# Optimization experiments

Measured on AMD Instinct MI355X. Metric: run time of the kernel, lower is better.

Reference implementation:

```python
import jax, jax.numpy as jnp
import numpy as np

TOP_K = 16
NUM_HEADS = 1
EPS = 1e-8  # torch F.cosine_similarity eps


def setup_inputs() -> dict:
    key = jax.random.key(0)
    ks = jax.random.split(key, 8)
    B, N, Dk, Dv = 64, 8192, 256, 256
    return {
        "query": jax.random.normal(ks[0], (B, Dk), jnp.float32),
        "key_memory": jax.random.normal(ks[1], (B, N, Dk), jnp.float32),
        "value_memory": jax.random.normal(ks[2], (B, N, Dv), jnp.float32),
        "iteration": jax.random.randint(ks[3], (B, 1), 0, N),
        "in_proj_w": jax.random.normal(ks[4], (3 * Dv, Dv), jnp.float32) * 0.06,
        "in_proj_b": jnp.zeros((3 * Dv,), jnp.float32),
        "out_proj_w": jax.random.normal(ks[5], (Dv, Dv), jnp.float32) * 0.06,
        "out_proj_b": jnp.zeros((Dv,), jnp.float32),
    }


def _mha(x, in_w, in_b, out_w, out_b):
    # torch nn.MultiheadAttention (batch_first, qkv same embed dim) self-attention
    B, T, E = x.shape
    H = NUM_HEADS
    hd = E // H
    qkv = x @ in_w.T + in_b                      # [B,T,3E]
    q, k, v = jnp.split(qkv, 3, axis=-1)

    def heads(t):
        return t.reshape(B, T, H, hd).transpose(0, 2, 1, 3)  # [B,H,T,hd]

    q, k, v = heads(q), heads(k), heads(v)
    scale = jnp.asarray(1.0 / np.sqrt(hd), x.dtype)
    attn = jax.nn.softmax(jnp.einsum('bhqd,bhkd->bhqk', q, k) * scale, axis=-1)
    o = jnp.einsum('bhqk,bhkd->bhqd', attn, v).transpose(0, 2, 1, 3).reshape(B, T, E)
    return o @ out_w.T + out_b


def reference(query, key_memory, value_memory, iteration,
              in_proj_w, in_proj_b, out_proj_w, out_proj_b):
    B, N, Dv = value_memory.shape
    # memory validity mask: item n is valid iff n <= iteration[b]
    mem_idx = jnp.arange(N)[None, :]                                   # [1,N]
    mask = (mem_idx <= iteration).astype(key_memory.dtype)[..., None]  # [B,N,1]
    km = key_memory * mask
    vm = value_memory * mask

    # masked cosine similarity between each memory key and the query
    num = jnp.einsum('bnd,bd->bn', km, query)                          # [B,N]
    denom = jnp.maximum(
        jnp.linalg.norm(km, axis=-1) * jnp.linalg.norm(query, axis=-1, keepdims=True),
        EPS)
    sim = num / denom                                                  # [B,N]

    topk_sim, topk_idx = jax.lax.top_k(sim, TOP_K)                     # [B,K]
    topk_vm = jnp.take_along_axis(vm, topk_idx[:, :, None], axis=1)    # [B,K,Dv]

    wv = jax.nn.softmax(topk_sim, axis=-1)[..., None]                  # [B,K,1]
    nrv = wv * topk_vm                                                 # [B,K,Dv]

    nrv = _mha(nrv, in_proj_w, in_proj_b, out_proj_w, out_proj_b)      # [B,K,Dv]

    # rows with iteration == 0 are left as zeros (scatter of computed rows)
    not_first = (iteration.reshape(-1) > 0).astype(nrv.dtype)[:, None, None]
    nrv = nrv * not_first
    return nrv.sum(axis=1)                                             # [B,Dv]
```

## Files before the change

### kernel.cpp

```cpp
#include <hip/hip_runtime.h>
#include <hip/hip_bf16.h>
#include <math.h>

#define B_   64
#define N_   8192
#define D_   256
#define K_   16
#define EPS_ 1e-8f
#define NEG_ -3.4e38f

static const size_t SIM_OFF   = 0;
static const size_t CANDV_OFF = 524288;
static const size_t CANDI_OFF = 655360;
static const size_t QKV_OFF   = 786432;

__global__ void __launch_bounds__(256)
sim_kernel(const float* __restrict__ q, const float* __restrict__ km,
           const int* __restrict__ iter, float* __restrict__ sim) {
    int tid = threadIdx.x;
    int w = tid >> 6, lane = tid & 63;
    int g = lane >> 4, p = lane & 15;
    int seg = (blockIdx.x << 2) + w;
    int b   = seg >> 7;
    int n0  = (seg & 127) << 6;
    int it  = iter[b];
    float* simb = sim + (size_t)b * N_;

    if (n0 > it) { simb[n0 + lane] = 0.f; return; }

    float4 q4[4];
    #pragma unroll
    for (int kk = 0; kk < 4; kk++)
        q4[kk] = *(const float4*)(q + (size_t)b * D_ + kk * 64 + p * 4);
    float qq = q4[0].x*q4[0].x + q4[0].y*q4[0].y + q4[0].z*q4[0].z + q4[0].w*q4[0].w
             + q4[1].x*q4[1].x + q4[1].y*q4[1].y + q4[1].z*q4[1].z + q4[1].w*q4[1].w
             + q4[2].x*q4[2].x + q4[2].y*q4[2].y + q4[2].z*q4[2].z + q4[2].w*q4[2].w
             + q4[3].x*q4[3].x + q4[3].y*q4[3].y + q4[3].z*q4[3].z + q4[3].w*q4[3].w;
    #pragma unroll
    for (int off = 8; off; off >>= 1) qq += __shfl_xor(qq, off);
    float qn = sqrtf(qq);

    const float* kmb = km + (size_t)b * N_ * D_;

    const float* rp0 = kmb + (size_t)min(n0 + g, it) * D_;
    float4 c0 = *(const float4*)(rp0 +   0 + p * 4);
    float4 c1 = *(const float4*)(rp0 +  64 + p * 4);
    float4 c2 = *(const float4*)(rp0 + 128 + p * 4);
    float4 c3 = *(const float4*)(rp0 + 192 + p * 4);

    for (int t = 0; t < 16; t++) {
        int r  = n0 + (t << 2) + g;
        int rn = (t < 15) ? (r + 4) : it;
        const float* rp = kmb + (size_t)min(rn, it) * D_;
        float4 x0 = *(const float4*)(rp +   0 + p * 4);
        float4 x1 = *(const float4*)(rp +  64 + p * 4);
        float4 x2 = *(const float4*)(rp + 128 + p * 4);
        float4 x3 = *(const float4*)(rp + 192 + p * 4);

        float dot = c0.x*q4[0].x + c0.y*q4[0].y + c0.z*q4[0].z + c0.w*q4[0].w
                  + c1.x*q4[1].x + c1.y*q4[1].y + c1.z*q4[1].z + c1.w*q4[1].w
                  + c2.x*q4[2].x + c2.y*q4[2].y + c2.z*q4[2].z + c2.w*q4[2].w
                  + c3.x*q4[3].x + c3.y*q4[3].y + c3.z*q4[3].z + c3.w*q4[3].w;
        float sq  = c0.x*c0.x + c0.y*c0.y + c0.z*c0.z + c0.w*c0.w
                  + c1.x*c1.x + c1.y*c1.y + c1.z*c1.z + c1.w*c1.w
                  + c2.x*c2.x + c2.y*c2.y + c2.z*c2.z + c2.w*c2.w
                  + c3.x*c3.x + c3.y*c3.y + c3.z*c3.z + c3.w*c3.w;
        #pragma unroll
        for (int off = 8; off; off >>= 1) {
            dot += __shfl_xor(dot, off);
            sq  += __shfl_xor(sq,  off);
        }
        float s = (r <= it) ? dot / fmaxf(sqrtf(sq) * qn, EPS_) : 0.f;
        if (p == 0) simb[r] = s;
        c0 = x0; c1 = x1; c2 = x2; c3 = x3;
    }
}

__global__ void __launch_bounds__(256)
cand_kernel(const float* __restrict__ sim,
            float* __restrict__ cand_v, int* __restrict__ cand_i) {
    int tid = threadIdx.x;
    int w = tid >> 6, lane = tid & 63;
    int seg = (blockIdx.x << 2) + w;
    int b   = seg >> 7;
    int n0  = (seg & 127) << 6;
    float v  = sim[(size_t)b * N_ + n0 + lane];
    int  idx = n0 + lane;
    #pragma unroll
    for (int k = 2; k <= 64; k <<= 1) {
        #pragma unroll
        for (int j = k >> 1; j > 0; j >>= 1) {
            float pv = __shfl_xor(v, j);
            int   pi = __shfl_xor(idx, j);
            bool up         = ((lane & k) == 0);
            bool is_lower   = ((lane & j) == 0);
            bool mine_first = (v > pv) || (v == pv && idx < pi);
            bool take_mine  = ((is_lower == up) == mine_first);
            if (!take_mine) { v = pv; idx = pi; }
        }
    }
    if (lane < K_) {
        cand_v[(size_t)seg * K_ + lane] = v;
        cand_i[(size_t)seg * K_ + lane] = idx;
    }
}

__global__ void __launch_bounds__(256)
merge_qkv_kernel(const float* __restrict__ cand_v, const int* __restrict__ cand_i,
                 const float* __restrict__ vm, const int* __restrict__ iter,
                 const float* __restrict__ inw, const float* __restrict__ inb,
                 float* __restrict__ qkv) {
    int bwh = blockIdx.x;
    int b = bwh / 3, which = bwh - b * 3;
    int tid = threadIdx.x, lane = tid & 63;
    int it = iter[b];
    if (it == 0) return;

    __shared__ int   seli[K_];
    __shared__ float scl[K_];
    __shared__ float xs[D_][K_];

    if (tid < 64) {
        float cv[32]; int ci[32];
        #pragma unroll
        for (int j = 0; j < 32; j++) {
            cv[j] = cand_v[(size_t)b * 2048 + (j << 6) + lane];
            ci[j] = cand_i[(size_t)b * 2048 + (j << 6) + lane];
        }
        float selv[K_]; int selidx[K_];
        for (int sel = 0; sel < K_; sel++) {
            float bv = cv[0]; int bi = ci[0];
            #pragma unroll
            for (int j = 1; j < 32; j++)
                if (cv[j] > bv || (cv[j] == bv && ci[j] < bi)) { bv = cv[j]; bi = ci[j]; }
            #pragma unroll
            for (int off = 32; off; off >>= 1) {
                float ov = __shfl_xor(bv, off);
                int   oi = __shfl_xor(bi, off);
                if (ov > bv || (ov == bv && oi < bi)) { bv = ov; bi = oi; }
            }
            #pragma unroll
            for (int j = 0; j < 32; j++)
                if (ci[j] == bi) cv[j] = NEG_;
            selv[sel] = bv; selidx[sel] = bi;
            if (lane == 0) seli[sel] = bi;
        }
        float m = NEG_;
        #pragma unroll
        for (int jj = 0; jj < K_; jj++) m = fmaxf(m, selv[jj]);
        float ssum = 0.f;
        #pragma unroll
        for (int jj = 0; jj < K_; jj++) ssum += expf(selv[jj] - m);
        if (lane < K_) {
            float wgt = expf(selv[lane] - m) / ssum;
            scl[lane] = (selidx[lane] <= it) ? wgt : 0.f;
        }
    }
    __syncthreads();

    #pragma unroll
    for (int kk = 0; kk < K_; kk += 4) {
        float4 px;
        px.x = scl[kk+0] * vm[((size_t)b * N_ + seli[kk+0]) * D_ + tid];
        px.y = scl[kk+1] * vm[((size_t)b * N_ + seli[kk+1]) * D_ + tid];
        px.z = scl[kk+2] * vm[((size_t)b * N_ + seli[kk+2]) * D_ + tid];
        px.w = scl[kk+3] * vm[((size_t)b * N_ + seli[kk+3]) * D_ + tid];
        *(float4*)(&xs[tid][kk]) = px;
    }
    __syncthreads();

    float acc[K_];
    #pragma unroll
    for (int k = 0; k < K_; k++) acc[k] = 0.f;
    const float* wrow = inw + (size_t)(which * D_ + tid) * D_;
    for (int d = 0; d < D_; d += 4) {
        float4 wv4 = *(const float4*)(wrow + d);
        float wk[4] = {wv4.x, wv4.y, wv4.z, wv4.w};
        #pragma unroll
        for (int dd = 0; dd < 4; dd++) {
            float wgt = wk[dd];
            float4 x0 = *(const float4*)(&xs[d + dd][0]);
            float4 x1 = *(const float4*)(&xs[d + dd][4]);
            float4 x2 = *(const float4*)(&xs[d + dd][8]);
            float4 x3 = *(const float4*)(&xs[d + dd][12]);
            acc[0]  += x0.x * wgt; acc[1]  += x0.y * wgt; acc[2]  += x0.z * wgt; acc[3]  += x0.w * wgt;
            acc[4]  += x1.x * wgt; acc[5]  += x1.y * wgt; acc[6]  += x1.z * wgt; acc[7]  += x1.w * wgt;
            acc[8]  += x2.x * wgt; acc[9]  += x2.y * wgt; acc[10] += x2.z * wgt; acc[11] += x2.w * wgt;
            acc[12] += x3.x * wgt; acc[13] += x3.y * wgt; acc[14] += x3.z * wgt; acc[15] += x3.w * wgt;
        }
    }
    float bias = inb[which * D_ + tid];
    #pragma unroll
    for (int k = 0; k < K_; k++)
        qkv[(((size_t)b * 3 + which) * K_ + k) * D_ + tid] = acc[k] + bias;
}

__global__ void __launch_bounds__(256)
attn_out_kernel(const float* __restrict__ qkv, const int* __restrict__ iter,
                const float* __restrict__ ow, const float* __restrict__ ob,
                float* __restrict__ out) {
    int b = blockIdx.x, tid = threadIdx.x;
    int it = iter[b];
    if (it == 0) { out[(size_t)b * D_ + tid] = 0.f; return; }
    __shared__ float qs[K_][260];
    __shared__ float ks[K_][260];
    __shared__ float vs[K_][260];
    __shared__ float attn[K_][K_];
    __shared__ float colsum[K_];
    __shared__ float so[D_];
    const float* base = qkv + (size_t)b * 3 * K_ * D_;
    #pragma unroll
    for (int k = 0; k < K_; k++) {
        qs[k][tid] = base[(0 * K_ + k) * D_ + tid];
        ks[k][tid] = base[(1 * K_ + k) * D_ + tid];
        vs[k][tid] = base[(2 * K_ + k) * D_ + tid];
    }
    __syncthreads();
    int i = tid >> 4, j = tid & 15;
    float s = 0.f;
    for (int d4 = 0; d4 < 64; d4++) {
        float4 qv = *(const float4*)(&qs[i][d4 * 4]);
        float4 kv = *(const float4*)(&ks[j][d4 * 4]);
        s += qv.x*kv.x + qv.y*kv.y + qv.z*kv.z + qv.w*kv.w;
    }
    attn[i][j] = s * 0.0625f;
    __syncthreads();
    if (tid < K_) {
        float m = NEG_;
        for (int jj = 0; jj < K_; jj++) m = fmaxf(m, attn[tid][jj]);
        float ssum = 0.f;
        for (int jj = 0; jj < K_; jj++) ssum += expf(attn[tid][jj] - m);
        float inv = 1.f / ssum;
        for (int jj = 0; jj < K_; jj++) attn[tid][jj] = expf(attn[tid][jj] - m) * inv;
    }
    __syncthreads();
    if (tid < K_) {
        float c = 0.f;
        for (int ii = 0; ii < K_; ii++) c += attn[ii][tid];
        colsum[tid] = c;
    }
    __syncthreads();
    float acc = 0.f;
    #pragma unroll
    for (int jj = 0; jj < K_; jj++) acc += colsum[jj] * vs[jj][tid];
    so[tid] = acc;
    __syncthreads();
    float o = 0.f;
    const float* orow = ow + (size_t)tid * D_;
    for (int e = 0; e < D_; e += 4) {
        float4 wv = *(const float4*)(orow + e);
        float4 sv = *(const float4*)(&so[e]);
        o += sv.x*wv.x + sv.y*wv.y + sv.z*wv.z + sv.w*wv.w;
    }
    out[(size_t)b * D_ + tid] = o + 16.f * ob[tid];
}

extern "C" void kernel_launch(void* const* d_in, const int* in_sizes, int n_in,
                              void* d_out, int out_size, void* d_ws, size_t ws_size,
                              hipStream_t stream) {
    const float* q   = (const float*)d_in[0];
    const float* km  = (const float*)d_in[1];
    const float* vm  = (const float*)d_in[2];
    const int*   it  = (const int*)  d_in[3];
    const float* inw = (const float*)d_in[4];
    const float* inb = (const float*)d_in[5];
    const float* ow  = (const float*)d_in[6];
    const float* ob  = (const float*)d_in[7];
    float* out = (float*)d_out;

    float* ws     = (float*)d_ws;
    float* sim    = ws + SIM_OFF;
    float* cand_v = ws + CANDV_OFF;
    int*   cand_i = (int*)(ws + CANDI_OFF);
    float* qkv    = ws + QKV_OFF;

    sim_kernel<<<dim3(2048), dim3(256), 0, stream>>>(q, km, it, sim);
    cand_kernel<<<dim3(2048), dim3(256), 0, stream>>>(sim, cand_v, cand_i);
    merge_qkv_kernel<<<dim3(B_ * 3), dim3(256), 0, stream>>>(cand_v, cand_i, vm, it, inw, inb, qkv);
    attn_out_kernel<<<dim3(B_), dim3(256), 0, stream>>>(qkv, it, ow, ob, out);
}
```

Measured before the change: 132.8 us.

## Process two key rows per group in sim kernel and split merge from QKV projection

The similarity kernel now handles two memory rows per 16-lane group in each iteration, with more loads in flight, and sets a minimum-occupancy launch bound. The top-k merge and value gather, which the old code ran redundantly in each of the three Q/K/V blocks, now run once per batch row in their own kernel that writes the scaled values to a workspace buffer. A separate QKV projection kernel then reads that buffer from global memory instead of shared memory. This removes the triplicated merge work and adds more memory-level parallelism, at the cost of an extra launch and a global round trip for the gathered values.

Measured after the change: 152.1 us. 14.6% more time.

```diff
diff --git a/kernel.cpp b/kernel.cpp
--- a/kernel.cpp
+++ b/kernel.cpp
@@ -12,9 +12,10 @@
 static const size_t SIM_OFF   = 0;
 static const size_t CANDV_OFF = 524288;
 static const size_t CANDI_OFF = 655360;
-static const size_t QKV_OFF   = 786432;
-
-__global__ void __launch_bounds__(256)
+static const size_t XBUF_OFF  = 786432;
+static const size_t QKV_OFF   = 1048576;
+
+__global__ void __launch_bounds__(256, 4)
 sim_kernel(const float* __restrict__ q, const float* __restrict__ km,
            const int* __restrict__ iter, float* __restrict__ sim) {
     int tid = threadIdx.x;
@@ -41,38 +42,57 @@
     float qn = sqrtf(qq);
 
     const float* kmb = km + (size_t)b * N_ * D_;
-
-    const float* rp0 = kmb + (size_t)min(n0 + g, it) * D_;
-    float4 c0 = *(const float4*)(rp0 +   0 + p * 4);
-    float4 c1 = *(const float4*)(rp0 +  64 + p * 4);
-    float4 c2 = *(const float4*)(rp0 + 128 + p * 4);
-    float4 c3 = *(const float4*)(rp0 + 192 + p * 4);
-
-    for (int t = 0; t < 16; t++) {
-        int r  = n0 + (t << 2) + g;
-        int rn = (t < 15) ? (r + 4) : it;
-        const float* rp = kmb + (size_t)min(rn, it) * D_;
-        float4 x0 = *(const float4*)(rp +   0 + p * 4);
-        float4 x1 = *(const float4*)(rp +  64 + p * 4);
-        float4 x2 = *(const float4*)(rp + 128 + p * 4);
-        float4 x3 = *(const float4*)(rp + 192 + p * 4);
-
-        float dot = c0.x*q4[0].x + c0.y*q4[0].y + c0.z*q4[0].z + c0.w*q4[0].w
-                  + c1.x*q4[1].x + c1.y*q4[1].y + c1.z*q4[1].z + c1.w*q4[1].w
-                  + c2.x*q4[2].x + c2.y*q4[2].y + c2.z*q4[2].z + c2.w*q4[2].w
-                  + c3.x*q4[3].x + c3.y*q4[3].y + c3.z*q4[3].z + c3.w*q4[3].w;
-        float sq  = c0.x*c0.x + c0.y*c0.y + c0.z*c0.z + c0.w*c0.w
-                  + c1.x*c1.x + c1.y*c1.y + c1.z*c1.z + c1.w*c1.w
-                  + c2.x*c2.x + c2.y*c2.y + c2.z*c2.z + c2.w*c2.w
-                  + c3.x*c3.x + c3.y*c3.y + c3.z*c3.z + c3.w*c3.w;
+    int p4 = p * 4;
+
+    float4 a0, a1, a2, a3, b0, b1, b2, b3;
+    {
+        int ra = n0 + (g << 1);
+        const float* pa = kmb + (size_t)min(ra,     it) * D_ + p4;
+        const float* pb = kmb + (size_t)min(ra + 1, it) * D_ + p4;
+        a0 = *(const float4*)(pa);       a1 = *(const float4*)(pa +  64);
+        a2 = *(const float4*)(pa + 128); a3 = *(const float4*)(pa + 192);
+        b0 = *(const float4*)(pb);       b1 = *(const float4*)(pb +  64);
+        b2 = *(const float4*)(pb + 128); b3 = *(const float4*)(pb + 192);
+    }
+
+    for (int t = 0; t < 8; t++) {
+        int ra = n0 + (t << 3) + (g << 1);
+        int nx = (t < 7) ? (ra + 8) : it;
+        const float* pa = kmb + (size_t)min(nx,     it) * D_ + p4;
+        const float* pb = kmb + (size_t)min(nx + 1, it) * D_ + p4;
+        float4 xa0 = *(const float4*)(pa);       float4 xa1 = *(const float4*)(pa +  64);
+        float4 xa2 = *(const float4*)(pa + 128); float4 xa3 = *(const float4*)(pa + 192);
+        float4 xb0 = *(const float4*)(pb);       float4 xb1 = *(const float4*)(pb +  64);
+        float4 xb2 = *(const float4*)(pb + 128); float4 xb3 = *(const float4*)(pb + 192);
+
+        float dota = a0.x*q4[0].x + a0.y*q4[0].y + a0.z*q4[0].z + a0.w*q4[0].w
+                   + a1.x*q4[1].x + a1.y*q4[1].y + a1.z*q4[1].z + a1.w*q4[1].w
+                   + a2.x*q4[2].x + a2.y*q4[2].y + a2.z*q4[2].z + a2.w*q4[2].w
+                   + a3.x*q4[3].x + a3.y*q4[3].y + a3.z*q4[3].z + a3.w*q4[3].w;
+        float sqa  = a0.x*a0.x + a0.y*a0.y + a0.z*a0.z + a0.w*a0.w
+                   + a1.x*a1.x + a1.y*a1.y + a1.z*a1.z + a1.w*a1.w
+                   + a2.x*a2.x + a2.y*a2.y + a2.z*a2.z + a2.w*a2.w
+                   + a3.x*a3.x + a3.y*a3.y + a3.z*a3.z + a3.w*a3.w;
+        float dotb = b0.x*q4[0].x + b0.y*q4[0].y + b0.z*q4[0].z + b0.w*q4[0].w
+                   + b1.x*q4[1].x + b1.y*q4[1].y + b1.z*q4[1].z + b1.w*q4[1].w
+                   + b2.x*q4[2].x + b2.y*q4[2].y + b2.z*q4[2].z + b2.w*q4[2].w
+                   + b3.x*q4[3].x + b3.y*q4[3].y + b3.z*q4[3].z + b3.w*q4[3].w;
+        float sqb  = b0.x*b0.x + b0.y*b0.y + b0.z*b0.z + b0.w*b0.w
+                   + b1.x*b1.x + b1.y*b1.y + b1.z*b1.z + b1.w*b1.w
+                   + b2.x*b2.x + b2.y*b2.y + b2.z*b2.z + b2.w*b2.w
+                   + b3.x*b3.x + b3.y*b3.y + b3.z*b3.z + b3.w*b3.w;
         #pragma unroll
         for (int off = 8; off; off >>= 1) {
-            dot += __shfl_xor(dot, off);
-            sq  += __shfl_xor(sq,  off);
-        }
-        float s = (r <= it) ? dot / fmaxf(sqrtf(sq) * qn, EPS_) : 0.f;
-        if (p == 0) simb[r] = s;
-        c0 = x0; c1 = x1; c2 = x2; c3 = x3;
+            dota += __shfl_xor(dota, off);
+            sqa  += __shfl_xor(sqa,  off);
+            dotb += __shfl_xor(dotb, off);
+            sqb  += __shfl_xor(sqb,  off);
+        }
+        float sa = (ra     <= it) ? dota / fmaxf(sqrtf(sqa) * qn, EPS_) : 0.f;
+        float sb = (ra + 1 <= it) ? dotb / fmaxf(sqrtf(sqb) * qn, EPS_) : 0.f;
+        if (p == 0) { simb[ra] = sa; simb[ra + 1] = sb; }
+        a0 = xa0; a1 = xa1; a2 = xa2; a3 = xa3;
+        b0 = xb0; b1 = xb1; b2 = xb2; b3 = xb3;
     }
 }
 
@@ -106,19 +126,16 @@
 }
 
 __global__ void __launch_bounds__(256)
-merge_qkv_kernel(const float* __restrict__ cand_v, const int* __restrict__ cand_i,
-                 const float* __restrict__ vm, const int* __restrict__ iter,
-                 const float* __restrict__ inw, const float* __restrict__ inb,
-                 float* __restrict__ qkv) {
-    int bwh = blockIdx.x;
-    int b = bwh / 3, which = bwh - b * 3;
+merge_gather_kernel(const float* __restrict__ cand_v, const int* __restrict__ cand_i,
+                    const float* __restrict__ vm, const int* __restrict__ iter,
+                    float* __restrict__ xbuf) {
+    int b = blockIdx.x;
     int tid = threadIdx.x, lane = tid & 63;
     int it = iter[b];
     if (it == 0) return;
 
     __shared__ int   seli[K_];
     __shared__ float scl[K_];
-    __shared__ float xs[D_][K_];
 
     if (tid < 64) {
         float cv[32]; int ci[32];
@@ -158,6 +175,7 @@
     }
     __syncthreads();
 
+    float* xb = xbuf + (size_t)b * (D_ * K_);
     #pragma unroll
     for (int kk = 0; kk < K_; kk += 4) {
         float4 px;
@@ -165,24 +183,35 @@
         px.y = scl[kk+1] * vm[((size_t)b * N_ + seli[kk+1]) * D_ + tid];
         px.z = scl[kk+2] * vm[((size_t)b * N_ + seli[kk+2]) * D_ + tid];
         px.w = scl[kk+3] * vm[((size_t)b * N_ + seli[kk+3]) * D_ + tid];
-        *(float4*)(&xs[tid][kk]) = px;
-    }
-    __syncthreads();
+        *(float4*)(xb + tid * K_ + kk) = px;
+    }
+}
+
+__global__ void __launch_bounds__(256)
+qkv_kernel(const float* __restrict__ xbuf, const int* __restrict__ iter,
+           const float* __restrict__ inw, const float* __restrict__ inb,
+           float* __restrict__ qkv) {
+    int bwh = blockIdx.x;
+    int b = bwh / 3, which = bwh - b * 3;
+    if (iter[b] == 0) return;
+    int tid = threadIdx.x;
 
     float acc[K_];
     #pragma unroll
     for (int k = 0; k < K_; k++) acc[k] = 0.f;
     const float* wrow = inw + (size_t)(which * D_ + tid) * D_;
+    const float* xb   = xbuf + (size_t)b * (D_ * K_);
     for (int d = 0; d < D_; d += 4) {
         float4 wv4 = *(const float4*)(wrow + d);
         float wk[4] = {wv4.x, wv4.y, wv4.z, wv4.w};
         #pragma unroll
         for (int dd = 0; dd < 4; dd++) {
             float wgt = wk[dd];
-            float4 x0 = *(const float4*)(&xs[d + dd][0]);
-            float4 x1 = *(const float4*)(&xs[d + dd][4]);
-            float4 x2 = *(const float4*)(&xs[d + dd][8]);
-            float4 x3 = *(const float4*)(&xs[d + dd][12]);
+            const float* xr = xb + (d + dd) * K_;
+            float4 x0 = *(const float4*)(xr);
+            float4 x1 = *(const float4*)(xr + 4);
+            float4 x2 = *(const float4*)(xr + 8);
+            float4 x3 = *(const float4*)(xr + 12);
             acc[0]  += x0.x * wgt; acc[1]  += x0.y * wgt; acc[2]  += x0.z * wgt; acc[3]  += x0.w * wgt;
             acc[4]  += x1.x * wgt; acc[5]  += x1.y * wgt; acc[6]  += x1.z * wgt; acc[7]  += x1.w * wgt;
             acc[8]  += x2.x * wgt; acc[9]  += x2.y * wgt; acc[10] += x2.z * wgt; acc[11] += x2.w * wgt;
@@ -272,10 +301,12 @@
     float* sim    = ws + SIM_OFF;
     float* cand_v = ws + CANDV_OFF;
     int*   cand_i = (int*)(ws + CANDI_OFF);
+    float* xbuf   = ws + XBUF_OFF;
     float* qkv    = ws + QKV_OFF;
 
     sim_kernel<<<dim3(2048), dim3(256), 0, stream>>>(q, km, it, sim);
     cand_kernel<<<dim3(2048), dim3(256), 0, stream>>>(sim, cand_v, cand_i);
-    merge_qkv_kernel<<<dim3(B_ * 3), dim3(256), 0, stream>>>(cand_v, cand_i, vm, it, inw, inb, qkv);
+    merge_gather_kernel<<<dim3(B_), dim3(256), 0, stream>>>(cand_v, cand_i, vm, it, xbuf);
+    qkv_kernel<<<dim3(B_ * 3), dim3(256), 0, stream>>>(xbuf, it, inw, inb, qkv);
     attn_out_kernel<<<dim3(B_), dim3(256), 0, stream>>>(qkv, it, ow, ob, out);
 }
```

## Use atomic work-stealing persistent waves for similarity computation

Applied to the files above, without the earlier changes.

Replaces the static one-wave-per-segment mapping in the similarity kernel with a persistent grid where each wave grabs segments from a global atomic counter. Segments are interleaved across batches so that the uneven, iteration-dependent work (segments beyond the valid range exit early) is spread evenly across waves. This adds an init kernel launch, atomic traffic, and a per-segment reload of the query vector.

Result: slower. 238.6 us (+79.7%).

```diff
diff --git a/kernel.cpp b/kernel.cpp
--- a/kernel.cpp
+++ b/kernel.cpp
@@ -6,6 +6,7 @@
 #define N_   8192
 #define D_   256
 #define K_   16
+#define NSEG_ 8192
 #define EPS_ 1e-8f
 #define NEG_ -3.4e38f
 
@@ -13,66 +14,80 @@
 static const size_t CANDV_OFF = 524288;
 static const size_t CANDI_OFF = 655360;
 static const size_t QKV_OFF   = 786432;
+static const size_t CTR_OFF   = 786432 + 786432;
+
+__global__ void init_kernel(int* __restrict__ ctr) {
+    if (threadIdx.x == 0) *ctr = 0;
+}
 
 __global__ void __launch_bounds__(256)
 sim_kernel(const float* __restrict__ q, const float* __restrict__ km,
-           const int* __restrict__ iter, float* __restrict__ sim) {
+           const int* __restrict__ iter, float* __restrict__ sim,
+           int* __restrict__ ctr) {
     int tid = threadIdx.x;
-    int w = tid >> 6, lane = tid & 63;
+    int lane = tid & 63;
     int g = lane >> 4, p = lane & 15;
-    int seg = (blockIdx.x << 2) + w;
-    int b   = seg >> 7;
-    int n0  = (seg & 127) << 6;
-    int it  = iter[b];
-    float* simb = sim + (size_t)b * N_;
-
-    if (n0 > it) { simb[n0 + lane] = 0.f; return; }
-
-    float4 q4[4];
-    #pragma unroll
-    for (int kk = 0; kk < 4; kk++)
-        q4[kk] = *(const float4*)(q + (size_t)b * D_ + kk * 64 + p * 4);
-    float qq = q4[0].x*q4[0].x + q4[0].y*q4[0].y + q4[0].z*q4[0].z + q4[0].w*q4[0].w
-             + q4[1].x*q4[1].x + q4[1].y*q4[1].y + q4[1].z*q4[1].z + q4[1].w*q4[1].w
-             + q4[2].x*q4[2].x + q4[2].y*q4[2].y + q4[2].z*q4[2].z + q4[2].w*q4[2].w
-             + q4[3].x*q4[3].x + q4[3].y*q4[3].y + q4[3].z*q4[3].z + q4[3].w*q4[3].w;
-    #pragma unroll
-    for (int off = 8; off; off >>= 1) qq += __shfl_xor(qq, off);
-    float qn = sqrtf(qq);
-
-    const float* kmb = km + (size_t)b * N_ * D_;
-
-    const float* rp0 = kmb + (size_t)min(n0 + g, it) * D_;
-    float4 c0 = *(const float4*)(rp0 +   0 + p * 4);
-    float4 c1 = *(const float4*)(rp0 +  64 + p * 4);
-    float4 c2 = *(const float4*)(rp0 + 128 + p * 4);
-    float4 c3 = *(const float4*)(rp0 + 192 + p * 4);
-
-    for (int t = 0; t < 16; t++) {
-        int r  = n0 + (t << 2) + g;
-        int rn = (t < 15) ? (r + 4) : it;
-        const float* rp = kmb + (size_t)min(rn, it) * D_;
-        float4 x0 = *(const float4*)(rp +   0 + p * 4);
-        float4 x1 = *(const float4*)(rp +  64 + p * 4);
-        float4 x2 = *(const float4*)(rp + 128 + p * 4);
-        float4 x3 = *(const float4*)(rp + 192 + p * 4);
-
-        float dot = c0.x*q4[0].x + c0.y*q4[0].y + c0.z*q4[0].z + c0.w*q4[0].w
-                  + c1.x*q4[1].x + c1.y*q4[1].y + c1.z*q4[1].z + c1.w*q4[1].w
-                  + c2.x*q4[2].x + c2.y*q4[2].y + c2.z*q4[2].z + c2.w*q4[2].w
-                  + c3.x*q4[3].x + c3.y*q4[3].y + c3.z*q4[3].z + c3.w*q4[3].w;
-        float sq  = c0.x*c0.x + c0.y*c0.y + c0.z*c0.z + c0.w*c0.w
-                  + c1.x*c1.x + c1.y*c1.y + c1.z*c1.z + c1.w*c1.w
-                  + c2.x*c2.x + c2.y*c2.y + c2.z*c2.z + c2.w*c2.w
-                  + c3.x*c3.x + c3.y*c3.y + c3.z*c3.z + c3.w*c3.w;
-        #pragma unroll
-        for (int off = 8; off; off >>= 1) {
-            dot += __shfl_xor(dot, off);
-            sq  += __shfl_xor(sq,  off);
-        }
-        float s = (r <= it) ? dot / fmaxf(sqrtf(sq) * qn, EPS_) : 0.f;
-        if (p == 0) simb[r] = s;
-        c0 = x0; c1 = x1; c2 = x2; c3 = x3;
+    int p4 = p * 4;
+
+    for (;;) {
+        int seg;
+        if (lane == 0) seg = atomicAdd(ctr, 1);
+        seg = __shfl(seg, 0);
+        if (seg >= NSEG_) return;
+
+        int b  = seg & 63;
+        int n0 = (seg >> 6) << 6;
+        int it = iter[b];
+        float* simb = sim + (size_t)b * N_;
+
+        if (n0 > it) { simb[n0 + lane] = 0.f; continue; }
+
+        float4 q4[4];
+        #pragma unroll
+        for (int kk = 0; kk < 4; kk++)
+            q4[kk] = *(const float4*)(q + (size_t)b * D_ + kk * 64 + p4);
+        float qq = q4[0].x*q4[0].x + q4[0].y*q4[0].y + q4[0].z*q4[0].z + q4[0].w*q4[0].w
+                 + q4[1].x*q4[1].x + q4[1].y*q4[1].y + q4[1].z*q4[1].z + q4[1].w*q4[1].w
+                 + q4[2].x*q4[2].x + q4[2].y*q4[2].y + q4[2].z*q4[2].z + q4[2].w*q4[2].w
+                 + q4[3].x*q4[3].x + q4[3].y*q4[3].y + q4[3].z*q4[3].z + q4[3].w*q4[3].w;
+        #pragma unroll
+        for (int off = 8; off; off >>= 1) qq += __shfl_xor(qq, off);
+        float qn = sqrtf(qq);
+
+        const float* kmb = km + (size_t)b * N_ * D_;
+
+        const float* rp0 = kmb + (size_t)min(n0 + g, it) * D_;
+        float4 c0 = *(const float4*)(rp0 +   0 + p4);
+        float4 c1 = *(const float4*)(rp0 +  64 + p4);
+        float4 c2 = *(const float4*)(rp0 + 128 + p4);
+        float4 c3 = *(const float4*)(rp0 + 192 + p4);
+
+        for (int t = 0; t < 16; t++) {
+            int r  = n0 + (t << 2) + g;
+            int rn = (t < 15) ? (r + 4) : it;
+            const float* rp = kmb + (size_t)min(rn, it) * D_;
+            float4 x0 = *(const float4*)(rp +   0 + p4);
+            float4 x1 = *(const float4*)(rp +  64 + p4);
+            float4 x2 = *(const float4*)(rp + 128 + p4);
+            float4 x3 = *(const float4*)(rp + 192 + p4);
+
+            float dot = c0.x*q4[0].x + c0.y*q4[0].y + c0.z*q4[0].z + c0.w*q4[0].w
+                      + c1.x*q4[1].x + c1.y*q4[1].y + c1.z*q4[1].z + c1.w*q4[1].w
+                      + c2.x*q4[2].x + c2.y*q4[2].y + c2.z*q4[2].z + c2.w*q4[2].w
+                      + c3.x*q4[3].x + c3.y*q4[3].y + c3.z*q4[3].z + c3.w*q4[3].w;
+            float sq  = c0.x*c0.x + c0.y*c0.y + c0.z*c0.z + c0.w*c0.w
+                      + c1.x*c1.x + c1.y*c1.y + c1.z*c1.z + c1.w*c1.w
+                      + c2.x*c2.x + c2.y*c2.y + c2.z*c2.z + c2.w*c2.w
+                      + c3.x*c3.x + c3.y*c3.y + c3.z*c3.z + c3.w*c3.w;
+            #pragma unroll
+            for (int off = 8; off; off >>= 1) {
+                dot += __shfl_xor(dot, off);
+                sq  += __shfl_xor(sq,  off);
+            }
+            float s = (r <= it) ? dot / fmaxf(sqrtf(sq) * qn, EPS_) : 0.f;
+            if (p == 0) simb[r] = s;
+            c0 = x0; c1 = x1; c2 = x2; c3 = x3;
+        }
     }
 }
 
@@ -273,8 +288,10 @@
     float* cand_v = ws + CANDV_OFF;
     int*   cand_i = (int*)(ws + CANDI_OFF);
     float* qkv    = ws + QKV_OFF;
-
-    sim_kernel<<<dim3(2048), dim3(256), 0, stream>>>(q, km, it, sim);
+    int*   ctr    = (int*)(ws + CTR_OFF);
+
+    init_kernel<<<dim3(1), dim3(64), 0, stream>>>(ctr);
+    sim_kernel<<<dim3(1024), dim3(256), 0, stream>>>(q, km, it, sim, ctr);
     cand_kernel<<<dim3(2048), dim3(256), 0, stream>>>(sim, cand_v, cand_i);
     merge_qkv_kernel<<<dim3(B_ * 3), dim3(256), 0, stream>>>(cand_v, cand_i, vm, it, inw, inb, qkv);
     attn_out_kernel<<<dim3(B_), dim3(256), 0, stream>>>(qkv, it, ow, ob, out);
```
